# Performance work log

Hardware: AMD Instinct MI355X
Metric: run time of the kernel (lower is better)

Reference implementation:

```python
import jax, jax.numpy as jnp
import numpy as np

N = 8192
K = 64    # k_neighbors


def setup_inputs() -> dict:
    key = jax.random.key(0)
    k1, k2 = jax.random.split(key)
    # Unique neighbor indices per row (topk of distances in the original module
    # guarantees uniqueness per row; we mimic that with argsort of random scores
    # so scatter-set semantics are well-defined/deterministic).
    scores = jax.random.uniform(k1, (N, N), dtype=jnp.float32)
    neighbor_indices = jnp.argsort(scores, axis=-1)[:, :K].astype(jnp.int32)  # [N, K]
    adjacency_values = jax.random.normal(k2, (N, K), dtype=jnp.float32)       # [N, K]
    return {"adjacency_values": adjacency_values, "neighbor_indices": neighbor_indices}


def reference(adjacency_values, neighbor_indices):
    # Vectorized equivalent of the per-row Python scatter loop:
    #   adjacency_full[i, neighbor_indices[i]] = adjacency_values[i]
    n, k = adjacency_values.shape
    rows = jnp.arange(n)[:, None]  # [N, 1] broadcast against [N, K] column indices
    adjacency_full = jnp.zeros((n, n), dtype=adjacency_values.dtype)
    return adjacency_full.at[rows, neighbor_indices].set(adjacency_values)
```

## Files before the change

kernel.cpp:

```cpp
#include <hip/hip_runtime.h>


constexpr int N_PATCH = 8192;
constexpr int K_NB = 64;
constexpr int BLOCK = 256;
constexpr int VEC_ITERS = N_PATCH / 4 / BLOCK;

__global__ __launch_bounds__(BLOCK)
void scatter_rows_kernel(const float* __restrict__ vals,
                         const int* __restrict__ idx,
                         float* __restrict__ out) {
    __shared__ float row[N_PATCH];
    const int r = blockIdx.x;
    const int t = threadIdx.x;

    float4* rowv = reinterpret_cast<float4*>(row);
    float4 z = make_float4(0.f, 0.f, 0.f, 0.f);
#pragma unroll
    for (int i = 0; i < VEC_ITERS; ++i)
        rowv[t + i * BLOCK] = z;
    __syncthreads();

    if (t < K_NB) {
        const int base = r * K_NB + t;
        const int c = idx[base];
        row[c] = vals[base];
    }
    __syncthreads();

    float4* outv = reinterpret_cast<float4*>(out + (size_t)r * N_PATCH);
#pragma unroll
    for (int i = 0; i < VEC_ITERS; ++i)
        outv[t + i * BLOCK] = rowv[t + i * BLOCK];
}

extern "C" void kernel_launch(void* const* d_in, const int* in_sizes, int n_in,
                              void* d_out, int out_size, void* d_ws, size_t ws_size,
                              hipStream_t stream) {
    const float* vals = (const float*)d_in[0];
    const int* idx = (const int*)d_in[1];
    float* out = (float*)d_out;

    scatter_rows_kernel<<<N_PATCH, BLOCK, 0, stream>>>(vals, idx, out);
}
```

Baseline: 259.3 us.

## Replace per-row LDS staging with memset plus direct scatter kernel

Zero the whole output with hipMemsetAsync and then launch a flat kernel where each thread writes one neighbor value straight to global memory. This removes the 32KB shared-memory row buffer, the two block barriers and the LDS round-trip, which limited occupancy and write bandwidth. In exchange it adds a second launch and scattered, uncoalesced single-float writes. It also relies on out_size being an element count.

```diff
diff --git a/kernel.cpp b/kernel.cpp
--- a/kernel.cpp
+++ b/kernel.cpp
@@ -3,35 +3,17 @@
 
 constexpr int N_PATCH = 8192;
 constexpr int K_NB = 64;
-constexpr int BLOCK = 256;
-constexpr int VEC_ITERS = N_PATCH / 4 / BLOCK;
+constexpr int TOTAL = N_PATCH * K_NB;
 
-__global__ __launch_bounds__(BLOCK)
-void scatter_rows_kernel(const float* __restrict__ vals,
-                         const int* __restrict__ idx,
-                         float* __restrict__ out) {
-    __shared__ float row[N_PATCH];
-    const int r = blockIdx.x;
-    const int t = threadIdx.x;
-
-    float4* rowv = reinterpret_cast<float4*>(row);
-    float4 z = make_float4(0.f, 0.f, 0.f, 0.f);
-#pragma unroll
-    for (int i = 0; i < VEC_ITERS; ++i)
-        rowv[t + i * BLOCK] = z;
-    __syncthreads();
-
-    if (t < K_NB) {
-        const int base = r * K_NB + t;
-        const int c = idx[base];
-        row[c] = vals[base];
-    }
-    __syncthreads();
-
-    float4* outv = reinterpret_cast<float4*>(out + (size_t)r * N_PATCH);
-#pragma unroll
-    for (int i = 0; i < VEC_ITERS; ++i)
-        outv[t + i * BLOCK] = rowv[t + i * BLOCK];
+__global__ __launch_bounds__(256)
+void scatter_kernel(const float* __restrict__ vals,
+                    const int* __restrict__ idx,
+                    float* __restrict__ out) {
+    const int f = blockIdx.x * 256 + threadIdx.x;
+    const int row = f >> 6;
+    const int col = idx[f];
+    const float v = vals[f];
+    out[(size_t)row * N_PATCH + col] = v;
 }
 
 extern "C" void kernel_launch(void* const* d_in, const int* in_sizes, int n_in,
@@ -41,5 +23,7 @@
     const int* idx = (const int*)d_in[1];
     float* out = (float*)d_out;
 
-    scatter_rows_kernel<<<N_PATCH, BLOCK, 0, stream>>>(vals, idx, out);
+    hipMemsetAsync(out, 0, (size_t)out_size * sizeof(float), stream);
+
+    scatter_kernel<<<TOTAL / 256, 256, 0, stream>>>(vals, idx, out);
 }
```

New measurement: 267.0 us. +2.9%, slower.
